# Kernel tuning notes

Hardware: AMD Instinct MI355X
Metric: run time of the kernel (lower is better)

Reference implementation:

```python
import jax, jax.numpy as jnp
import numpy as np
from functools import partial

TAU = 2.0
BN_EPS = 1e-5
SG_ALPHA = 4.0  # spikingjelly surrogate.Sigmoid default

@jax.custom_vjp
def heaviside(x):
    return (x >= 0.0).astype(x.dtype)

def _heaviside_fwd(x):
    return heaviside(x), x

def _heaviside_bwd(x, g):
    s = jax.nn.sigmoid(SG_ALPHA * x)
    return (g * SG_ALPHA * s * (1.0 - s),)

heaviside.defvjp(_heaviside_fwd, _heaviside_bwd)

def lif(x_seq, v_threshold=1.0):
    # MultiStepLIFNode: tau=2, decay_input=True, v_reset=0 (hard reset), detach_reset
    def step(v, x):
        v = v + (x - v) / TAU
        s = heaviside(v - v_threshold)
        v = v * (1.0 - jax.lax.stop_gradient(s))
        return v, s
    _, s_seq = jax.lax.scan(step, jnp.zeros_like(x_seq[0]), x_seq)
    return s_seq

def conv1x1_bn(x, w, gamma, beta, mean, var, b=None):
    # x: [T,B,C,N]; w: [Cout,Cin]; 1x1 conv == channel matmul; BN in eval mode
    y = jnp.einsum('oc,tbcn->tbon', w, x)
    if b is not None:
        y = y + b[:, None]
    inv = gamma / jnp.sqrt(var + BN_EPS)
    return y * inv[:, None] + (beta - mean * inv)[:, None]

def setup_inputs() -> dict:
    key = jax.random.key(0)
    ks = jax.random.split(key, 24)
    T, B, C, N = 4, 32, 384, 196
    d = {}
    d['x'] = jax.random.normal(ks[0], (T, B, C, N), dtype=jnp.float32)
    d['policy'] = jax.random.uniform(ks[1], (T * B, N, 1), dtype=jnp.float32)
    scale = 1.0 / np.sqrt(C)
    for i, p in enumerate(['q', 'k', 'v', 'proj']):
        base = 2 + i * 5
        d[p + '_w'] = jax.random.normal(ks[base], (C, C), dtype=jnp.float32) * scale
        d[p + '_gamma'] = jnp.ones((C,), jnp.float32)
        d[p + '_beta'] = jnp.zeros((C,), jnp.float32)
        d[p + '_mean'] = jax.random.normal(ks[base + 1], (C,), dtype=jnp.float32) * 0.1
        d[p + '_var'] = jax.random.uniform(ks[base + 2], (C,), dtype=jnp.float32, minval=0.5, maxval=1.5)
    d['proj_b'] = jnp.zeros((C,), jnp.float32)
    return d

def _to_heads(s, H):
    T, B, C, N = s.shape
    # [T,B,C,N] -> [T,B,N,H,D] -> [T,B,H,N,D]
    return s.transpose(0, 1, 3, 2).reshape(T, B, N, H, C // H).transpose(0, 1, 3, 2, 4)

def reference(x, policy, q_w, q_gamma, q_beta, q_mean, q_var,
              k_w, k_gamma, k_beta, k_mean, k_var,
              v_w, v_gamma, v_beta, v_mean, v_var,
              proj_w, proj_gamma, proj_beta, proj_mean, proj_var, proj_b):
    T, B, C, N = x.shape
    H = 12
    attn_scale = 0.25
    q = _to_heads(lif(conv1x1_bn(x, q_w, q_gamma, q_beta, q_mean, q_var)), H)
    k = _to_heads(lif(conv1x1_bn(x, k_w, k_gamma, k_beta, k_mean, k_var)), H)
    v = _to_heads(lif(conv1x1_bn(x, v_w, v_gamma, v_beta, v_mean, v_var)), H)
    attn = jnp.einsum('tbhnd,tbhmd->tbhnm', q, k)
    # attention_policy: attn *= (policy + (1-policy)*eye)
    pol = policy.reshape(T, B, 1, 1, N)
    eye = jnp.eye(N, dtype=attn.dtype)
    attn = attn * (pol + (1.0 - pol) * eye)
    y = jnp.einsum('tbhnm,tbhmd->tbhnd', attn, v) * attn_scale
    y = y.transpose(0, 1, 2, 4, 3).reshape(T, B, C, N)
    y = lif(y, v_threshold=0.5)
    y = conv1x1_bn(y, proj_w, proj_gamma, proj_beta, proj_mean, proj_var, b=proj_b)
    return lif(y)
```

## Files before the change

### kernel.cpp

```cpp
#include <hip/hip_runtime.h>

typedef unsigned int u32;
typedef __bf16 bf16x8 __attribute__((ext_vector_type(8)));
typedef __bf16 bf16x4v __attribute__((ext_vector_type(4)));
typedef _Float16 f16x8 __attribute__((ext_vector_type(8)));
typedef float f32x4 __attribute__((ext_vector_type(4)));

#define Tn 4
#define Bn 32
#define Cn 384
#define Nn 196
#define Hn 12
#define CNn (Cn*Nn)
#define BCNn (Bn*CNn)
#define BHNn (Bn*Hn*Nn)
#define PBITS (Tn*BHNn)
#define TBCNn (Tn*BCNn)
#define NCOLS 6272
#define WSZ 147456

__device__ __forceinline__ void split3(float v, __bf16& h, __bf16& m, __bf16& l) {
  h = (__bf16)v;  float r = v - (float)h;
  m = (__bf16)r;  float r2 = r - (float)m;
  l = (__bf16)r2;
}
__device__ __forceinline__ void split2h(float v, _Float16& h, _Float16& l) {
  h = (_Float16)v;  l = (_Float16)(v - (float)h);
}

__device__ __forceinline__ void gl_lds16(const void* g, void* l) {
  __builtin_amdgcn_global_load_lds(
      (const __attribute__((address_space(1))) unsigned int*)g,
      (__attribute__((address_space(3))) unsigned int*)l, 16, 0, 0);
}

struct WSplitArgs {
  const float* w[4]; const float* g[4]; const float* be[4];
  const float* mu[4]; const float* va[4]; const float* bias;
};
__global__ __launch_bounds__(256) void split_w(
    WSplitArgs a, _Float16* __restrict__ wsp16, __bf16* __restrict__ wspb,
    float* __restrict__ shv) {
  const int i = blockIdx.x * 256 + threadIdx.x;
  const int p = i / WSZ, r = i - p * WSZ;
  const int o = r / Cn;
  const float iv = a.g[p][o] / sqrtf(a.va[p][o] + 1e-5f);
  const float wv = a.w[p][r] * iv;
  if (p < 3) {
    _Float16 h, l;
    split2h(wv, h, l);
    wsp16[(size_t)(p * 2 + 0) * WSZ + r] = h;
    wsp16[(size_t)(p * 2 + 1) * WSZ + r] = l;
  } else {
    __bf16 h, m, l;
    split3(wv, h, m, l);
    wspb[(size_t)0 * WSZ + r] = h;
    wspb[(size_t)1 * WSZ + r] = m;
    wspb[(size_t)2 * WSZ + r] = l;
  }
  if (r - o * Cn == 0) {
    float sh = a.be[p][o] - a.mu[p][o] * iv;
    if (p == 3) sh += a.bias[o] * iv;
    shv[p * Cn + o] = sh;
  }
}

__global__ __launch_bounds__(256) void transpose_split_x(
    const float* __restrict__ x, _Float16* __restrict__ xs) {
  __shared__ float tile[49 * 130];
  const int t = blockIdx.x, b = blockIdx.y;
  const int ct = blockIdx.z >> 2, nch = blockIdx.z & 3;
  const int c0 = ct * 128, n0 = nch * 49;
  const int tid = threadIdx.x;
  for (int idx = tid; idx < 49 * 128; idx += 256) {
    const int n = idx % 49, c = idx / 49;
    tile[n * 130 + c] = x[(size_t)t * BCNn + (size_t)b * CNn +
                          (size_t)(c0 + c) * Nn + n0 + n];
  }
  __syncthreads();
  for (int idx = tid; idx < 49 * 64; idx += 256) {
    const int cp = idx & 63, n = idx >> 6;
    const float v0 = tile[n * 130 + cp * 2];
    const float v1 = tile[n * 130 + cp * 2 + 1];
    _Float16 h0, l0, h1, l1;
    split2h(v0, h0, l0);
    split2h(v1, h1, l1);
    const size_t col = (size_t)t * NCOLS + (size_t)b * Nn + n0 + n;
    union { _Float16 f[2]; u32 u; } uh, ul;
    uh.f[0] = h0; uh.f[1] = h1;
    ul.f[0] = l0; ul.f[1] = l1;
    ((u32*)(xs + col * Cn + c0))[cp] = uh.u;
    ((u32*)(xs + (size_t)TBCNn + col * Cn + c0))[cp] = ul.u;
  }
}

__global__ __launch_bounds__(256, 2) void gemm_qkv_lif(
    const _Float16* __restrict__ xs,
    const _Float16* __restrict__ wsp16,
    const float* __restrict__ shv,
    u32* __restrict__ bq, u32* __restrict__ bk, u32* __restrict__ bv)
{
  __shared__ _Float16 Asw[3][2][128][32];
  __shared__ _Float16 Bsw[3][2][64][32];
  const int orig = blockIdx.x;
  const int xcd = orig & 7, i8 = orig >> 3;
  const int wgid = xcd * 110 + (xcd < 2 ? xcd : 2) + i8;
  const int colt = wgid / 9, v = wgid - colt * 9;
  const int col0 = colt * 64;
  const int p = v / 3, mt = v - p * 3;
  const int o0 = mt * 128;
  const int tid = threadIdx.x, lane = tid & 63, wid = tid >> 6;
  const int wm = wid >> 1, wn = wid & 1;
  const int quad = lane >> 4, nl = lane & 15;
  u32* __restrict__ bits = (p == 0) ? bq : (p == 1) ? bk : bv;

  u32 aOff[4], bOff[2];
#pragma unroll
  for (int i = 0; i < 4; ++i) {
    const int c = i * 256 + wid * 64 + lane;
    const int s = c >> 9, row = (c >> 2) & 127, kb = c & 3;
    const int kbs = kb ^ ((row >> 1) & 3);
    aOff[i] = (u32)((((p * 2 + s) * WSZ) + (o0 + row) * Cn + kbs * 8) * 2);
  }
#pragma unroll
  for (int i = 0; i < 2; ++i) {
    const int c = i * 256 + wid * 64 + lane;
    const int s = c >> 8, rem = c & 255, row = rem >> 2, kb = rem & 3;
    const int kbs = kb ^ ((row >> 1) & 3);
    bOff[i] = (u32)(((size_t)s * TBCNn + (size_t)(col0 + row) * Cn + kbs * 8) * 2);
  }
  const char* wB = (const char*)wsp16;
  const char* xB = (const char*)xs;
  char* aD0 = (char*)&Asw[0][0][0][0] + wid * 1024;
  char* bD0 = (char*)&Bsw[0][0][0][0] + wid * 1024;

#define STAGE_QKV(s_, buf_) do {                                          \
    const int t_ = (s_) / 12, kk_ = (s_) - t_ * 12;                       \
    const u32 ak_ = (u32)(kk_ * 64);                                      \
    const u32 bk_ = ak_ + (u32)t_ * (u32)(NCOLS * Cn * 2);                \
    _Pragma("unroll") for (int i_ = 0; i_ < 4; ++i_)                      \
      gl_lds16(wB + aOff[i_] + ak_, aD0 + (buf_) * 16384 + i_ * 4096);    \
    _Pragma("unroll") for (int i_ = 0; i_ < 2; ++i_)                      \
      gl_lds16(xB + bOff[i_] + bk_, bD0 + (buf_) * 8192 + i_ * 4096);     \
  } while (0)

  f32x4 sh_[4];
#pragma unroll
  for (int mi = 0; mi < 4; ++mi)
    sh_[mi] = *(const f32x4*)&shv[p * Cn + o0 + wm * 64 + mi * 16 + quad * 4];

  f32x4 acc[4][2];
  f32x4 vst[4][2] = {};

  STAGE_QKV(0, 0);
  STAGE_QKV(1, 1);

#pragma unroll 1
  for (int s = 0; s < 48; ++s) {
    const int kk = s % 12;
    const int buf = s % 3;
    if (s < 47) asm volatile("s_waitcnt vmcnt(6)" ::: "memory");
    else        asm volatile("s_waitcnt vmcnt(0)" ::: "memory");
    __builtin_amdgcn_s_barrier();
    __builtin_amdgcn_sched_barrier(0);
    if (s + 2 < 48) STAGE_QKV(s + 2, (s + 2) % 3);
    if (kk == 0) {
#pragma unroll
      for (int mi = 0; mi < 4; ++mi)
#pragma unroll
        for (int ni = 0; ni < 2; ++ni) acc[mi][ni] = f32x4{0.f, 0.f, 0.f, 0.f};
    }
    f16x8 bfr[2][2];
#pragma unroll
    for (int i = 0; i < 2; ++i) {
      const int rb = wn * 32 + i * 16 + nl;
      const int kb2 = (quad ^ ((rb >> 1) & 3)) * 8;
#pragma unroll
      for (int sp_ = 0; sp_ < 2; ++sp_)
        bfr[sp_][i] = *(const f16x8*)&Bsw[buf][sp_][rb][kb2];
    }
#pragma unroll
    for (int mi = 0; mi < 4; ++mi) {
      const int ra = wm * 64 + mi * 16 + nl;
      const int ka = (quad ^ ((ra >> 1) & 3)) * 8;
      const f16x8 a0 = *(const f16x8*)&Asw[buf][0][ra][ka];
      const f16x8 a1 = *(const f16x8*)&Asw[buf][1][ra][ka];
#pragma unroll
      for (int ni = 0; ni < 2; ++ni) {
        f32x4 c = acc[mi][ni];
        c = __builtin_amdgcn_mfma_f32_16x16x32_f16(a0, bfr[0][ni], c, 0, 0, 0);
        c = __builtin_amdgcn_mfma_f32_16x16x32_f16(a0, bfr[1][ni], c, 0, 0, 0);
        c = __builtin_amdgcn_mfma_f32_16x16x32_f16(a1, bfr[0][ni], c, 0, 0, 0);
        acc[mi][ni] = c;
      }
    }
    if (kk == 11) {
      const int t = s / 12;
#pragma unroll
      for (int ni = 0; ni < 2; ++ni) {
        u32 w0 = 0, w1 = 0;
#pragma unroll
        for (int mi = 0; mi < 4; ++mi) {
#pragma unroll
          for (int r = 0; r < 4; ++r) {
            const float y = acc[mi][ni][r] + sh_[mi][r];
            const float vv = vst[mi][ni][r];
            const float nv = vv + (y - vv) * 0.5f;
            const bool sk = nv >= 1.0f;
            vst[mi][ni][r] = sk ? 0.f : nv;
            const u32 b1 = sk ? 1u : 0u;
            const int pos = ((mi & 1) << 4) + (quad << 2) + r;
            if (mi < 2) w0 |= b1 << pos; else w1 |= b1 << pos;
          }
        }
        w0 |= __shfl_xor(w0, 16); w0 |= __shfl_xor(w0, 32);
        w1 |= __shfl_xor(w1, 16); w1 |= __shfl_xor(w1, 32);
        if (quad == 0) {
          const int col = col0 + wn * 32 + ni * 16 + nl;
          const int bb = col / Nn, nn = col - bb * Nn;
          u32* bp = bits + (size_t)t * BHNn +
                    ((size_t)bb * Hn + (mt * 4 + wm * 2)) * Nn + nn;
          bp[0] = w0;
          bp[Nn] = w1;
        }
      }
    }
  }
#undef STAGE_QKV
}

#define ASTR 40
__global__ __launch_bounds__(256) void attn_lif(
    const u32* __restrict__ qb, const u32* __restrict__ kb,
    const u32* __restrict__ vb, const float* __restrict__ policy,
    __bf16* __restrict__ sp) {
  __shared__ u32 qs[208], ks[224], vs_[224];
  __shared__ float ps[224];
  __shared__ __bf16 psp[3][224];
  __shared__ __bf16 Al[208 * ASTR];
  __shared__ __bf16 Ul[3][32 * ASTR];
  const int bh = blockIdx.x;
  const int bN = bh / Hn;
  const int h = bh - bN * Hn;
  const int tid = threadIdx.x;
  const int lane = tid & 63, wid = tid >> 6;
  const int quad = lane >> 4, nl = lane & 15;

  float vst[4][2][4] = {};

  for (int t = 0; t < Tn; ++t) {
    const int tb = t * Bn + bN;
    const int gid = tb * Hn + h;
    if (t) __syncthreads();
    for (int i = tid; i < 224; i += 256) {
      const bool in = i < Nn;
      if (i < 208) qs[i] = in ? qb[(size_t)gid * Nn + i] : 0u;
      ks[i] = in ? kb[(size_t)gid * Nn + i] : 0u;
      vs_[i] = in ? vb[(size_t)gid * Nn + i] : 0u;
      const float p = in ? policy[(size_t)tb * Nn + i] : 0.f;
      ps[i] = p;
      __bf16 hh, mm, ll;
      split3(p, hh, mm, ll);
      psp[0][i] = hh; psp[1][i] = mm; psp[2][i] = ll;
    }
    __syncthreads();

    f32x4 acc[4][2] = {};

    for (int slab = 0; slab < 7; ++slab) {
      const int m0 = slab * 32;
      if (tid < 208) {
        const u32 qn = qs[tid];
        __bf16 a32[32];
#pragma unroll
        for (int mk = 0; mk < 32; ++mk)
          a32[mk] = (__bf16)(float)__popc(qn & ks[m0 + mk]);
#pragma unroll
        for (int g = 0; g < 4; ++g)
          *(bf16x8*)&Al[tid * ASTR + g * 8] = *(bf16x8*)&a32[g * 8];
      }
      {
        const int dp = tid >> 3, mkg = (tid & 7) * 4;
        __bf16 u4[3][4];
#pragma unroll
        for (int j = 0; j < 4; ++j) {
          const int m = m0 + mkg + j;
          const bool bit = (vs_[m] >> dp) & 1u;
#pragma unroll
          for (int s = 0; s < 3; ++s)
            u4[s][j] = bit ? psp[s][m] : (__bf16)0.f;
        }
#pragma unroll
        for (int s = 0; s < 3; ++s)
          *(bf16x4v*)&Ul[s][dp * ASTR + mkg] = *(bf16x4v*)u4[s];
      }
      __syncthreads();
      bf16x8 bfr[3][2];
#pragma unroll
      for (int s = 0; s < 3; ++s)
#pragma unroll
        for (int nt = 0; nt < 2; ++nt)
          bfr[s][nt] = *(const bf16x8*)&Ul[s][(nt * 16 + nl) * ASTR + quad * 8];
#pragma unroll
      for (int mi = 0; mi < 4; ++mi) {
        const int mt2 = wid + mi * 4;
        if (mt2 < 13) {
          const bf16x8 af = *(const bf16x8*)&Al[(mt2 * 16 + nl) * ASTR + quad * 8];
#pragma unroll
          for (int nt = 0; nt < 2; ++nt) {
            f32x4 c = acc[mi][nt];
            c = __builtin_amdgcn_mfma_f32_16x16x32_bf16(af, bfr[0][nt], c, 0, 0, 0);
            c = __builtin_amdgcn_mfma_f32_16x16x32_bf16(af, bfr[1][nt], c, 0, 0, 0);
            c = __builtin_amdgcn_mfma_f32_16x16x32_bf16(af, bfr[2][nt], c, 0, 0, 0);
            acc[mi][nt] = c;
          }
        }
      }
      __syncthreads();
    }
#pragma unroll
    for (int mi = 0; mi < 4; ++mi) {
      const int mt2 = wid + mi * 4;
      if (mt2 >= 13) continue;
#pragma unroll
      for (int r = 0; r < 4; ++r) {
        const int n = mt2 * 16 + quad * 4 + r;
        if (n >= Nn) continue;
        const float ann = (float)__popc(qs[n] & ks[n]);
        const float wd = ann * (1.0f - ps[n]);
        const u32 vn = vs_[n];
        __bf16* op = sp + (size_t)t * BCNn + ((size_t)bN * Nn + n) * Cn + h * 32;
#pragma unroll
        for (int nt = 0; nt < 2; ++nt) {
          const int d = nt * 16 + nl;
          const float bit = (float)((vn >> d) & 1u);
          const float y = (acc[mi][nt][r] + wd * bit) * 0.25f;
          const float vv = vst[mi][nt][r];
          const float nv = vv + (y - vv) * 0.5f;
          const bool s = nv >= 0.5f;
          vst[mi][nt][r] = s ? 0.f : nv;
          op[d] = (__bf16)(s ? 1.0f : 0.0f);
        }
      }
    }
  }
}

__global__ __launch_bounds__(256, 3) void gemm_proj_mfma(
    const __bf16* __restrict__ sp, const __bf16* __restrict__ wspb,
    const float* __restrict__ shv, float* __restrict__ z)
{
  __shared__ __bf16 Asw[3][128][32];
  __shared__ __bf16 Bsw[128][32];
  const int bid = blockIdx.x;
  const int xcd = bid & 7, slot = bid >> 3;
  const int gl = slot / 3, mt = slot - gl * 3;
  const int group = xcd * 25 + gl;
  if (group >= 196) return;
  const int colt = group % 49, t = group / 49;
  const int col0 = colt * 128, o0 = mt * 128;
  const int tid = threadIdx.x, lane = tid & 63, wid = tid >> 6;
  const int wm = wid >> 1, wn = wid & 1;
  const int quad = lane >> 4, nl = lane & 15;
  const __bf16* Bg = sp + ((size_t)t * NCOLS + col0) * Cn;

  f32x4 acc[4][4] = {};
  bf16x8 aval[6], bval[2];
#pragma unroll
  for (int i = 0; i < 6; ++i) {
    const int u = tid + i * 256, s = u >> 9, rem = u & 511;
    const int row = rem >> 2, kb = rem & 3;
    aval[i] = *(const bf16x8*)(wspb + (size_t)s * WSZ + (size_t)(o0 + row) * Cn + kb * 8);
  }
#pragma unroll
  for (int i = 0; i < 2; ++i) {
    const int u = tid + i * 256, row = u >> 2, kb = u & 3;
    bval[i] = *(const bf16x8*)(Bg + (size_t)row * Cn + kb * 8);
  }

  for (int kk = 0; kk < 12; ++kk) {
    __syncthreads();
#pragma unroll
    for (int i = 0; i < 6; ++i) {
      const int u = tid + i * 256, s = u >> 9, rem = u & 511;
      const int row = rem >> 2, kb = rem & 3;
      const int kbp = kb ^ ((row >> 1) & 3);
      *(bf16x8*)&Asw[s][row][kbp * 8] = aval[i];
    }
#pragma unroll
    for (int i = 0; i < 2; ++i) {
      const int u = tid + i * 256, row = u >> 2, kb = u & 3;
      const int kbp = kb ^ ((row >> 1) & 3);
      *(bf16x8*)&Bsw[row][kbp * 8] = bval[i];
    }
    __syncthreads();
    if (kk < 11) {
      const int k0n = (kk + 1) * 32;
#pragma unroll
      for (int i = 0; i < 6; ++i) {
        const int u = tid + i * 256, s = u >> 9, rem = u & 511;
        const int row = rem >> 2, kb = rem & 3;
        aval[i] = *(const bf16x8*)(wspb + (size_t)s * WSZ +
                                   (size_t)(o0 + row) * Cn + k0n + kb * 8);
      }
#pragma unroll
      for (int i = 0; i < 2; ++i) {
        const int u = tid + i * 256, row = u >> 2, kb = u & 3;
        bval[i] = *(const bf16x8*)(Bg + (size_t)row * Cn + k0n + kb * 8);
      }
    }
    bf16x8 af[3][4], bfr[4];
#pragma unroll
    for (int i = 0; i < 4; ++i) {
      const int ra = wm * 64 + i * 16 + nl;
      const int rb = wn * 64 + i * 16 + nl;
      const int ka = (quad ^ ((ra >> 1) & 3)) * 8;
      const int kb2 = (quad ^ ((rb >> 1) & 3)) * 8;
      bfr[i] = *(const bf16x8*)&Bsw[rb][kb2];
#pragma unroll
      for (int s = 0; s < 3; ++s)
        af[s][i] = *(const bf16x8*)&Asw[s][ra][ka];
    }
#pragma unroll
    for (int mi = 0; mi < 4; ++mi)
#pragma unroll
      for (int ni = 0; ni < 4; ++ni) {
        f32x4 c = acc[mi][ni];
        c = __builtin_amdgcn_mfma_f32_16x16x32_bf16(af[0][mi], bfr[ni], c, 0, 0, 0);
        c = __builtin_amdgcn_mfma_f32_16x16x32_bf16(af[1][mi], bfr[ni], c, 0, 0, 0);
        c = __builtin_amdgcn_mfma_f32_16x16x32_bf16(af[2][mi], bfr[ni], c, 0, 0, 0);
        acc[mi][ni] = c;
      }
  }
#pragma unroll
  for (int mi = 0; mi < 4; ++mi) {
    const int ob = o0 + wm * 64 + mi * 16 + quad * 4;
    const f32x4 sh4 = *(const f32x4*)&shv[3 * Cn + ob];
#pragma unroll
    for (int ni = 0; ni < 4; ++ni) {
      const int col = col0 + wn * 64 + ni * 16 + nl;
      const int b = col / Nn, nn = col - b * Nn;
      float* zp = z + (size_t)t * BCNn + (size_t)b * CNn + nn;
#pragma unroll
      for (int r = 0; r < 4; ++r)
        zp[(size_t)(ob + r) * Nn] = acc[mi][ni][r] + sh4[r];
    }
  }
}

__global__ __launch_bounds__(256) void lif_out_v4(
    const float* __restrict__ z, float* __restrict__ out) {
  const size_t i4 = ((size_t)blockIdx.x * 256 + threadIdx.x) * 4;
  f32x4 v = {0.f, 0.f, 0.f, 0.f};
#pragma unroll
  for (int t = 0; t < Tn; ++t) {
    f32x4 x = *(const f32x4*)(z + (size_t)t * BCNn + i4);
    f32x4 o4;
#pragma unroll
    for (int r = 0; r < 4; ++r) {
      const float nv = v[r] + (x[r] - v[r]) * 0.5f;
      const bool s = nv >= 1.0f;
      o4[r] = s ? 1.0f : 0.0f;
      v[r] = s ? 0.f : nv;
    }
    *(f32x4*)(out + (size_t)t * BCNn + i4) = o4;
  }
}

extern "C" void kernel_launch(void* const* d_in, const int* in_sizes, int n_in,
                              void* d_out, int out_size, void* d_ws, size_t ws_size,
                              hipStream_t stream) {
  const float* x      = (const float*)d_in[0];
  const float* policy = (const float*)d_in[1];
  const float* qw = (const float*)d_in[2];
  const float* qg = (const float*)d_in[3];
  const float* qb_ = (const float*)d_in[4];
  const float* qm = (const float*)d_in[5];
  const float* qv = (const float*)d_in[6];
  const float* kw = (const float*)d_in[7];
  const float* kg = (const float*)d_in[8];
  const float* kbe = (const float*)d_in[9];
  const float* km = (const float*)d_in[10];
  const float* kv = (const float*)d_in[11];
  const float* vw = (const float*)d_in[12];
  const float* vg = (const float*)d_in[13];
  const float* vbe = (const float*)d_in[14];
  const float* vm = (const float*)d_in[15];
  const float* vv = (const float*)d_in[16];
  const float* pw = (const float*)d_in[17];
  const float* pg = (const float*)d_in[18];
  const float* pbe = (const float*)d_in[19];
  const float* pm = (const float*)d_in[20];
  const float* pv = (const float*)d_in[21];
  const float* pbias = (const float*)d_in[22];
  float* out = (float*)d_out;

  char* base = (char*)d_ws;
  _Float16* xs   = (_Float16*)base;
  _Float16* wsp16 = (_Float16*)(base + (size_t)TBCNn * 4);
  __bf16* wspb   = (__bf16*)((char*)wsp16 + (size_t)6 * WSZ * 2);
  float* shv     = (float*)((char*)wspb + (size_t)3 * WSZ * 2);
  u32* bq        = (u32*)((char*)shv + 4 * Cn * 4);
  u32* bk = bq + PBITS;
  u32* bv = bk + PBITS;
  __bf16* sp     = (__bf16*)(bv + PBITS);
  float* z       = (float*)((char*)sp + (size_t)TBCNn * 2);

  WSplitArgs wa;
  wa.w[0] = qw; wa.g[0] = qg; wa.be[0] = qb_; wa.mu[0] = qm; wa.va[0] = qv;
  wa.w[1] = kw; wa.g[1] = kg; wa.be[1] = kbe; wa.mu[1] = km; wa.va[1] = kv;
  wa.w[2] = vw; wa.g[2] = vg; wa.be[2] = vbe; wa.mu[2] = vm; wa.va[2] = vv;
  wa.w[3] = pw; wa.g[3] = pg; wa.be[3] = pbe; wa.mu[3] = pm; wa.va[3] = pv;
  wa.bias = pbias;
  split_w<<<2304, 256, 0, stream>>>(wa, wsp16, wspb, shv);
  transpose_split_x<<<dim3(4, 32, 12), 256, 0, stream>>>(x, xs);

  gemm_qkv_lif<<<882, 256, 0, stream>>>(xs, wsp16, shv, bq, bk, bv);
  attn_lif<<<Bn * Hn, 256, 0, stream>>>(bq, bk, bv, policy, sp);
  gemm_proj_mfma<<<600, 256, 0, stream>>>(sp, wspb, shv, z);
  lif_out_v4<<<BCNn / 1024, 256, 0, stream>>>(z, out);
}
```

Baseline: 317.6 us.

## Share QKV weight tiles across timestep pairs in the spike GEMM

The QKV projection loop now processes two timesteps together. Each staged weight (A) tile is loaded from LDS into registers once and reused against the activation (B) tiles of both timesteps. That halves weight staging and LDS reads per MFMA, with separate ring buffers and wait counts for the A and B streams. The LIF epilogue runs for both timesteps in order, and MFMA blocks are wrapped in s_setprio. The cost is a second accumulator set, which raises register pressure and could lower occupancy.

```diff
diff --git a/kernel.cpp b/kernel.cpp
--- a/kernel.cpp
+++ b/kernel.cpp
@@ -134,14 +134,19 @@
   char* aD0 = (char*)&Asw[0][0][0][0] + wid * 1024;
   char* bD0 = (char*)&Bsw[0][0][0][0] + wid * 1024;
 
-#define STAGE_QKV(s_, buf_) do {                                          \
-    const int t_ = (s_) / 12, kk_ = (s_) - t_ * 12;                       \
-    const u32 ak_ = (u32)(kk_ * 64);                                      \
-    const u32 bk_ = ak_ + (u32)t_ * (u32)(NCOLS * Cn * 2);                \
-    _Pragma("unroll") for (int i_ = 0; i_ < 4; ++i_)                      \
-      gl_lds16(wB + aOff[i_] + ak_, aD0 + (buf_) * 16384 + i_ * 4096);    \
-    _Pragma("unroll") for (int i_ = 0; i_ < 2; ++i_)                      \
-      gl_lds16(xB + bOff[i_] + bk_, bD0 + (buf_) * 8192 + i_ * 4096);     \
+#define STAGE_A(ai_) do {                                                  \
+    const u32 ak_ = (u32)(((ai_) % 12) * 64);                              \
+    char* d_ = aD0 + ((ai_) % 3) * 16384;                                  \
+    _Pragma("unroll") for (int i_ = 0; i_ < 4; ++i_)                       \
+      gl_lds16(wB + aOff[i_] + ak_, d_ + i_ * 4096);                       \
+  } while (0)
+#define STAGE_B(g_) do {                                                   \
+    const int t_ = ((g_) / 24) * 2 + ((g_) & 1);                           \
+    const int kk_ = (((g_) % 24) >> 1);                                    \
+    const u32 bk_ = (u32)(kk_ * 64) + (u32)t_ * (u32)(NCOLS * Cn * 2);     \
+    char* d_ = bD0 + ((g_) % 3) * 8192;                                    \
+    _Pragma("unroll") for (int i_ = 0; i_ < 2; ++i_)                       \
+      gl_lds16(xB + bOff[i_] + bk_, d_ + i_ * 4096);                       \
   } while (0)
 
   f32x4 sh_[4];
@@ -149,84 +154,129 @@
   for (int mi = 0; mi < 4; ++mi)
     sh_[mi] = *(const f32x4*)&shv[p * Cn + o0 + wm * 64 + mi * 16 + quad * 4];
 
-  f32x4 acc[4][2];
+  f32x4 acc0[4][2], acc1[4][2];
   f32x4 vst[4][2] = {};
 
-  STAGE_QKV(0, 0);
-  STAGE_QKV(1, 1);
+  auto epi = [&](f32x4 (&ac)[4][2], int t) {
+#pragma unroll
+    for (int ni = 0; ni < 2; ++ni) {
+      u32 w0 = 0, w1 = 0;
+#pragma unroll
+      for (int mi = 0; mi < 4; ++mi) {
+#pragma unroll
+        for (int r = 0; r < 4; ++r) {
+          const float y = ac[mi][ni][r] + sh_[mi][r];
+          const float vv = vst[mi][ni][r];
+          const float nv = vv + (y - vv) * 0.5f;
+          const bool sk = nv >= 1.0f;
+          vst[mi][ni][r] = sk ? 0.f : nv;
+          const u32 b1 = sk ? 1u : 0u;
+          const int pos = ((mi & 1) << 4) + (quad << 2) + r;
+          if (mi < 2) w0 |= b1 << pos; else w1 |= b1 << pos;
+        }
+      }
+      w0 |= __shfl_xor(w0, 16); w0 |= __shfl_xor(w0, 32);
+      w1 |= __shfl_xor(w1, 16); w1 |= __shfl_xor(w1, 32);
+      if (quad == 0) {
+        const int col = col0 + wn * 32 + ni * 16 + nl;
+        const int bb = col / Nn, nn = col - bb * Nn;
+        u32* bp = bits + (size_t)t * BHNn +
+                  ((size_t)bb * Hn + (mt * 4 + wm * 2)) * Nn + nn;
+        bp[0] = w0;
+        bp[Nn] = w1;
+      }
+    }
+  };
+
+  STAGE_B(0); STAGE_A(0); STAGE_B(1); STAGE_A(1);
 
 #pragma unroll 1
-  for (int s = 0; s < 48; ++s) {
-    const int kk = s % 12;
-    const int buf = s % 3;
-    if (s < 47) asm volatile("s_waitcnt vmcnt(6)" ::: "memory");
-    else        asm volatile("s_waitcnt vmcnt(0)" ::: "memory");
+  for (int gg = 0; gg < 24; ++gg) {
+    const int abuf = gg % 3;
+    const int be = (2 * gg) % 3, bo = (2 * gg + 1) % 3;
+    const int kk = gg % 12;
+
+    if (gg < 23) { asm volatile("s_waitcnt vmcnt(6)" ::: "memory"); }
+    else         { asm volatile("s_waitcnt vmcnt(2)" ::: "memory"); }
     __builtin_amdgcn_s_barrier();
     __builtin_amdgcn_sched_barrier(0);
-    if (s + 2 < 48) STAGE_QKV(s + 2, (s + 2) % 3);
+    if (gg < 23) STAGE_B(2 * gg + 2);
     if (kk == 0) {
 #pragma unroll
       for (int mi = 0; mi < 4; ++mi)
 #pragma unroll
-        for (int ni = 0; ni < 2; ++ni) acc[mi][ni] = f32x4{0.f, 0.f, 0.f, 0.f};
-    }
-    f16x8 bfr[2][2];
-#pragma unroll
-    for (int i = 0; i < 2; ++i) {
-      const int rb = wn * 32 + i * 16 + nl;
-      const int kb2 = (quad ^ ((rb >> 1) & 3)) * 8;
-#pragma unroll
-      for (int sp_ = 0; sp_ < 2; ++sp_)
-        bfr[sp_][i] = *(const f16x8*)&Bsw[buf][sp_][rb][kb2];
-    }
+        for (int ni = 0; ni < 2; ++ni) {
+          acc0[mi][ni] = f32x4{0.f, 0.f, 0.f, 0.f};
+          acc1[mi][ni] = f32x4{0.f, 0.f, 0.f, 0.f};
+        }
+    }
+    f16x8 af0[4], af1[4];
 #pragma unroll
     for (int mi = 0; mi < 4; ++mi) {
       const int ra = wm * 64 + mi * 16 + nl;
       const int ka = (quad ^ ((ra >> 1) & 3)) * 8;
-      const f16x8 a0 = *(const f16x8*)&Asw[buf][0][ra][ka];
-      const f16x8 a1 = *(const f16x8*)&Asw[buf][1][ra][ka];
-#pragma unroll
-      for (int ni = 0; ni < 2; ++ni) {
-        f32x4 c = acc[mi][ni];
-        c = __builtin_amdgcn_mfma_f32_16x16x32_f16(a0, bfr[0][ni], c, 0, 0, 0);
-        c = __builtin_amdgcn_mfma_f32_16x16x32_f16(a0, bfr[1][ni], c, 0, 0, 0);
-        c = __builtin_amdgcn_mfma_f32_16x16x32_f16(a1, bfr[0][ni], c, 0, 0, 0);
-        acc[mi][ni] = c;
-      }
+      af0[mi] = *(const f16x8*)&Asw[abuf][0][ra][ka];
+      af1[mi] = *(const f16x8*)&Asw[abuf][1][ra][ka];
+    }
+    {
+      f16x8 bfr[2][2];
+#pragma unroll
+      for (int i = 0; i < 2; ++i) {
+        const int rb = wn * 32 + i * 16 + nl;
+        const int kb2 = (quad ^ ((rb >> 1) & 3)) * 8;
+        bfr[0][i] = *(const f16x8*)&Bsw[be][0][rb][kb2];
+        bfr[1][i] = *(const f16x8*)&Bsw[be][1][rb][kb2];
+      }
+      __builtin_amdgcn_s_setprio(1);
+#pragma unroll
+      for (int mi = 0; mi < 4; ++mi)
+#pragma unroll
+        for (int ni = 0; ni < 2; ++ni) {
+          f32x4 c = acc0[mi][ni];
+          c = __builtin_amdgcn_mfma_f32_16x16x32_f16(af0[mi], bfr[0][ni], c, 0, 0, 0);
+          c = __builtin_amdgcn_mfma_f32_16x16x32_f16(af0[mi], bfr[1][ni], c, 0, 0, 0);
+          c = __builtin_amdgcn_mfma_f32_16x16x32_f16(af1[mi], bfr[0][ni], c, 0, 0, 0);
+          acc0[mi][ni] = c;
+        }
+      __builtin_amdgcn_s_setprio(0);
+    }
+
+    if (gg < 23) { asm volatile("s_waitcnt vmcnt(6)" ::: "memory"); }
+    else         { asm volatile("s_waitcnt vmcnt(0)" ::: "memory"); }
+    __builtin_amdgcn_s_barrier();
+    __builtin_amdgcn_sched_barrier(0);
+    if (gg < 23) STAGE_B(2 * gg + 3);
+    if (gg < 22) STAGE_A(gg + 2);
+    {
+      f16x8 bfr[2][2];
+#pragma unroll
+      for (int i = 0; i < 2; ++i) {
+        const int rb = wn * 32 + i * 16 + nl;
+        const int kb2 = (quad ^ ((rb >> 1) & 3)) * 8;
+        bfr[0][i] = *(const f16x8*)&Bsw[bo][0][rb][kb2];
+        bfr[1][i] = *(const f16x8*)&Bsw[bo][1][rb][kb2];
+      }
+      __builtin_amdgcn_s_setprio(1);
+#pragma unroll
+      for (int mi = 0; mi < 4; ++mi)
+#pragma unroll
+        for (int ni = 0; ni < 2; ++ni) {
+          f32x4 c = acc1[mi][ni];
+          c = __builtin_amdgcn_mfma_f32_16x16x32_f16(af0[mi], bfr[0][ni], c, 0, 0, 0);
+          c = __builtin_amdgcn_mfma_f32_16x16x32_f16(af0[mi], bfr[1][ni], c, 0, 0, 0);
+          c = __builtin_amdgcn_mfma_f32_16x16x32_f16(af1[mi], bfr[0][ni], c, 0, 0, 0);
+          acc1[mi][ni] = c;
+        }
+      __builtin_amdgcn_s_setprio(0);
     }
     if (kk == 11) {
-      const int t = s / 12;
-#pragma unroll
-      for (int ni = 0; ni < 2; ++ni) {
-        u32 w0 = 0, w1 = 0;
-#pragma unroll
-        for (int mi = 0; mi < 4; ++mi) {
-#pragma unroll
-          for (int r = 0; r < 4; ++r) {
-            const float y = acc[mi][ni][r] + sh_[mi][r];
-            const float vv = vst[mi][ni][r];
-            const float nv = vv + (y - vv) * 0.5f;
-            const bool sk = nv >= 1.0f;
-            vst[mi][ni][r] = sk ? 0.f : nv;
-            const u32 b1 = sk ? 1u : 0u;
-            const int pos = ((mi & 1) << 4) + (quad << 2) + r;
-            if (mi < 2) w0 |= b1 << pos; else w1 |= b1 << pos;
-          }
-        }
-        w0 |= __shfl_xor(w0, 16); w0 |= __shfl_xor(w0, 32);
-        w1 |= __shfl_xor(w1, 16); w1 |= __shfl_xor(w1, 32);
-        if (quad == 0) {
-          const int col = col0 + wn * 32 + ni * 16 + nl;
-          const int bb = col / Nn, nn = col - bb * Nn;
-          u32* bp = bits + (size_t)t * BHNn +
-                    ((size_t)bb * Hn + (mt * 4 + wm * 2)) * Nn + nn;
-          bp[0] = w0;
-          bp[Nn] = w1;
-        }
-      }
-    }
-  }
-#undef STAGE_QKV
+      const int p2 = gg / 12;
+      epi(acc0, p2 * 2 + 0);
+      epi(acc1, p2 * 2 + 1);
+    }
+  }
+#undef STAGE_A
+#undef STAGE_B
 }
 
 #define ASTR 40
```

After: 307.6 us. 1.03x faster.
